# Optimization experiments

Hardware: AMD Instinct MI355X
Metric: run time of the kernel (lower is better)

The kernel has to match this reference:

```python
import jax, jax.numpy as jnp
import numpy as np

ANG = 5
WS = 8
HEADS = 2
REF = 2  # refPos = [2, 2]
NEG_SLOPE = 0.1
EPS = 1e-5


def _rel_pos_index(ws):
    coords = np.stack(np.meshgrid(np.arange(ws), np.arange(ws), indexing='ij'))  # [2,ws,ws]
    cf = coords.reshape(2, -1)
    rel = (cf[:, :, None] - cf[:, None, :]).transpose(1, 2, 0)  # [N,N,2]
    rel[..., 0] += ws - 1
    rel[..., 1] += ws - 1
    rel[..., 0] *= 2 * ws - 1
    return jnp.asarray(rel.sum(-1))  # [N,N] int

REL_IDX = _rel_pos_index(WS)


def _ln(x, g, b):
    m = jnp.mean(x, -1, keepdims=True)
    v = jnp.var(x, -1, keepdims=True)
    return (x - m) * jax.lax.rsqrt(v + EPS) * g + b


def setup_inputs():
    key = jax.random.key(0)
    ks = jax.random.split(key, 12)
    b, an2, c, h, w = 2, 25, 32, 96, 96
    C = 2 * c
    s = 0.02
    mlp_hidden = int(C * 4.0)
    inp = {}
    inp['global_fea'] = jax.random.normal(ks[0], (b, an2, c, h, w), jnp.float32)
    inp['centra_fea'] = jax.random.normal(ks[1], (b, c, h, w), jnp.float32)
    inp['disparity'] = jax.random.uniform(ks[2], (b, 1, h, w), jnp.float32)
    inp['qkv_w'] = jax.random.normal(ks[3], (3 * C, C), jnp.float32) * s
    inp['qkv_b'] = jnp.zeros((3 * C,), jnp.float32)
    inp['proj_w'] = jax.random.normal(ks[4], (C, C), jnp.float32) * s
    inp['proj_b'] = jnp.zeros((C,), jnp.float32)
    inp['rpb_table'] = jax.random.normal(ks[5], ((2 * WS - 1) ** 2, HEADS), jnp.float32) * s
    inp['ln1_g'] = jnp.ones((C,), jnp.float32)
    inp['ln1_b'] = jnp.zeros((C,), jnp.float32)
    inp['ln2_g'] = jnp.ones((C,), jnp.float32)
    inp['ln2_b'] = jnp.zeros((C,), jnp.float32)
    inp['fc1_w'] = jax.random.normal(ks[6], (mlp_hidden, C), jnp.float32) * s
    inp['fc1_b'] = jnp.zeros((mlp_hidden,), jnp.float32)
    inp['fc2_w'] = jax.random.normal(ks[7], (C, mlp_hidden), jnp.float32) * s
    inp['fc2_b'] = jnp.zeros((C,), jnp.float32)
    inp['conv_w'] = jax.random.normal(ks[8], (c, C), jnp.float32) * s  # 1x1 conv kernel squeezed
    inp['conv_b'] = jnp.zeros((c,), jnp.float32)
    return inp


def _warp(centra_fea, disparity):
    # back-projection: bilinear warp of the central (2,2) view to all ANG*ANG views
    b, c, h, w = centra_fea.shape
    d = disparity[:, 0]  # [b,h,w]
    ys, xs = jnp.meshgrid(jnp.arange(h, dtype=jnp.float32), jnp.arange(w, dtype=jnp.float32), indexing='ij')
    offs = jnp.asarray([[u - REF, v - REF] for u in range(ANG) for v in range(ANG)], jnp.float32)  # [an2,2]
    sy = ys[None, None] + d[:, None] * offs[None, :, 0, None, None]  # [b,an2,h,w]
    sx = xs[None, None] + d[:, None] * offs[None, :, 1, None, None]
    x0f = jnp.floor(sx)
    y0f = jnp.floor(sy)
    wx = sx - x0f
    wy = sy - y0f
    x0 = jnp.clip(x0f.astype(jnp.int32), 0, w - 1)
    x1 = jnp.clip(x0 + 1, 0, w - 1)
    y0 = jnp.clip(y0f.astype(jnp.int32), 0, h - 1)
    y1 = jnp.clip(y0 + 1, 0, h - 1)
    flat = centra_fea.reshape(b, c, h * w)
    an2 = ANG * ANG

    def gather(yi, xi):
        idx = (yi * w + xi).reshape(b, 1, -1)  # [b,1,an2*h*w]
        g = jnp.take_along_axis(flat, jnp.broadcast_to(idx, (b, c, an2 * h * w)), axis=2)
        return g.reshape(b, c, an2, h, w).transpose(0, 2, 1, 3, 4)  # [b,an2,c,h,w]

    wx_ = wx[:, :, None]
    wy_ = wy[:, :, None]
    return ((1 - wy_) * (1 - wx_) * gather(y0, x0) + (1 - wy_) * wx_ * gather(y0, x1)
            + wy_ * (1 - wx_) * gather(y1, x0) + wy_ * wx_ * gather(y1, x1))


def reference(global_fea, centra_fea, disparity, qkv_w, qkv_b, proj_w, proj_b, rpb_table,
              ln1_g, ln1_b, ln2_g, ln2_b, fc1_w, fc1_b, fc2_w, fc2_b, conv_w, conv_b):
    b, an2, c, h, w = global_fea.shape
    warped = _warp(centra_fea, disparity)
    x = jnp.concatenate([global_fea, warped], axis=2)  # [b,an2,2c,h,w]
    C = 2 * c
    B = b * an2
    # 'b an2 c h w -> (b an2) (h w) c'
    x = x.reshape(B, C, h, w).transpose(0, 2, 3, 1).reshape(B, h * w, C)
    # --- Swin transformer block (shift_size=0, iteration_idx=0) ---
    shortcut = x
    xn = _ln(x, ln1_g, ln1_b).reshape(B, h, w, C)
    nh, nw = h // WS, w // WS
    xw = xn.reshape(B, nh, WS, nw, WS, C).transpose(0, 1, 3, 2, 4, 5).reshape(B * nh * nw, WS * WS, C)
    nwins, N = xw.shape[0], WS * WS
    hd = C // HEADS
    qkv = (xw @ qkv_w.T + qkv_b).reshape(nwins, N, 3, HEADS, hd).transpose(2, 0, 3, 1, 4)
    q, k, v = qkv[0], qkv[1], qkv[2]  # [nwins, heads, N, hd]
    scale = hd ** -0.5
    attn = jnp.einsum('whnd,whmd->whnm', q * scale, k)
    bias = rpb_table[REL_IDX].transpose(2, 0, 1)  # [heads,N,N]
    attn = jax.nn.softmax(attn + bias[None], axis=-1)
    out = jnp.einsum('whnm,whmd->whnd', attn, v).transpose(0, 2, 1, 3).reshape(nwins, N, C)
    out = out @ proj_w.T + proj_b
    out = out.reshape(B, nh, nw, WS, WS, C).transpose(0, 1, 3, 2, 4, 5).reshape(B, h * w, C)
    x = shortcut + out
    xm = _ln(x, ln2_g, ln2_b)
    xm = jax.nn.gelu(xm @ fc1_w.T + fc1_b, approximate=False) @ fc2_w.T + fc2_b
    x = x + xm
    # '(b an2) (h w) c -> (b an2) c h w' then 1x1 conv fuse + LeakyReLU(0.1)
    x = x.reshape(B, h, w, C)
    y = jnp.einsum('bhwc,oc->bohw', x, conv_w) + conv_b[None, :, None, None]
    y = jnp.where(y >= 0, y, NEG_SLOPE * y)
    return y.reshape(b, an2, c, h, w)
```

## Files before the change

kernel.cpp:

```cpp
#include <hip/hip_runtime.h>
#include <hip/hip_bf16.h>
#include <math.h>

#define W_    96
#define HW_   9216
#define NWIN_ 144

typedef __attribute__((ext_vector_type(4))) float          f32x4;
typedef __attribute__((ext_vector_type(8))) __bf16         bf16x8;
typedef __attribute__((ext_vector_type(8))) unsigned short u16x8;

#define MFMA(a,b,c) __builtin_amdgcn_mfma_f32_16x16x32_bf16((a),(b),(c),0,0,0)

#define WOFF_QKV  0
#define WOFF_PROJ 12288
#define WOFF_FC1  16384
#define WOFF_FC2  32768
#define WOFF_CONV 49152
#define WTOT      51200
#define BIAS_N    8192
#define POFF_QKVB  0
#define POFF_PROJB 192
#define POFF_FC1B  256
#define POFF_FC2B  512
#define POFF_CONVB 576
#define POFF_LN1G  1058
#define POFF_LN1B  1122
#define POFF_LN2G  1186
#define POFF_LN2B  1250
#define PTOT       1314

#define LOG2E 1.44269504f

__device__ __forceinline__ float ldin(const void* p, long i, int isbf){
    return isbf ? __bfloat162float(((const __hip_bfloat16*)p)[i]) : ((const float*)p)[i];
}
__device__ __forceinline__ bf16x8 ldbf8(const __bf16* w){
    u16x8 u = *(const u16x8*)w;
    return __builtin_bit_cast(bf16x8, u);
}

__device__ __forceinline__ float gelu_f(float v){
    float t = v*v;
    float s = 2.3022151f + 0.10294372f*t;
    float z = __builtin_amdgcn_exp2f(fminf(v*s, 80.f));
    return v*z*__builtin_amdgcn_rcpf(z + 1.f);
}

__global__ void probe_kernel(const void* ln1g, int* flag){
    if (threadIdx.x == 0){
        unsigned u = *(const unsigned*)ln1g;
        *flag = (u == 0x3F803F80u) ? 1 : 0;
    }
}

__global__ __launch_bounds__(256) void convert_params(
    const int* __restrict__ flag,
    const void* qkvw, const void* qkvb, const void* projw, const void* projb, const void* rpb,
    const void* ln1g, const void* ln1b, const void* ln2g, const void* ln2b,
    const void* fc1w, const void* fc1b, const void* fc2w, const void* fc2b,
    const void* convw, const void* convb,
    __bf16* __restrict__ wbf, float* __restrict__ pf, float* __restrict__ biasf)
{
    const int isbf = *flag;
    int idx = blockIdx.x*256 + threadIdx.x;
    if (idx >= WTOT + PTOT + BIAS_N) return;
    if (idx < WTOT){
        if      (idx < 12288) wbf[WOFF_QKV  + idx]          = (__bf16)ldin(qkvw, idx, isbf);
        else if (idx < 16384) wbf[WOFF_PROJ + (idx-12288)]  = (__bf16)ldin(projw, idx-12288, isbf);
        else if (idx < 32768) wbf[WOFF_FC1  + (idx-16384)]  = (__bf16)ldin(fc1w, idx-16384, isbf);
        else if (idx < 49152) wbf[WOFF_FC2  + (idx-32768)]  = (__bf16)ldin(fc2w, idx-32768, isbf);
        else                  wbf[WOFF_CONV + (idx-49152)]  = (__bf16)ldin(convw, idx-49152, isbf);
    } else if (idx < WTOT + PTOT){
        int p = idx - WTOT;
        if      (p < 192)  pf[POFF_QKVB  + p]        = ldin(qkvb, p, isbf);
        else if (p < 256)  pf[POFF_PROJB + (p-192)]  = ldin(projb, p-192, isbf);
        else if (p < 512)  pf[POFF_FC1B  + (p-256)]  = ldin(fc1b, p-256, isbf);
        else if (p < 576)  pf[POFF_FC2B  + (p-512)]  = ldin(fc2b, p-512, isbf);
        else if (p < 608)  pf[POFF_CONVB + (p-576)]  = ldin(convb, p-576, isbf);
        else if (p < 1058) ;
        else if (p < 1122) pf[POFF_LN1G  + (p-1058)] = ldin(ln1g, p-1058, isbf);
        else if (p < 1186) pf[POFF_LN1B  + (p-1122)] = ldin(ln1b, p-1122, isbf);
        else if (p < 1250) pf[POFF_LN2G  + (p-1186)] = ldin(ln2g, p-1186, isbf);
        else               pf[POFF_LN2B  + (p-1250)] = ldin(ln2b, p-1250, isbf);
    } else {
        int eb = idx - (WTOT + PTOT);
        int r = eb & 3, jt = (eb>>2)&3, h = (eb>>4)&1, cl = (eb>>5)&15, g = (eb>>9)&3, w = (eb>>11)&3;
        int i = w*16 + g*4 + r;
        int j = jt*16 + cl;
        int di = (i>>3)-(j>>3)+7, dj = (i&7)-(j&7)+7;
        biasf[eb] = ldin(rpb, (di*15+dj)*2 + h, isbf) * LOG2E;
    }
}

template<typename T>
__device__ __forceinline__ void phaseA(
    const T* __restrict__ gf, const T* __restrict__ cf, const T* __restrict__ disp,
    float* tile, float* tile2,
    int tid,int b,int a,int wy,int wx,int hw00)
{
    const int p = tid & 63;
    const int ty = p >> 3, tx = p & 7;
    const int y = wy*8 + ty, x = wx*8 + tx;
    float d = (float)disp[(long)b*HW_ + y*W_ + x];
    float dy = (float)(a/5 - 2), dxs = (float)(a%5 - 2);
    float sy = (float)y + d*dy, sx = (float)x + d*dxs;
    float y0f = floorf(sy), x0f = floorf(sx);
    float fy = sy - y0f, fx = sx - x0f;
    int y0 = min(max((int)y0f,0), W_-1);
    int x0 = min(max((int)x0f,0), W_-1);
    int y1 = min(y0+1,W_-1), x1 = min(x0+1,W_-1);
    float w00=(1.f-fy)*(1.f-fx), w01=(1.f-fy)*fx, w10=fy*(1.f-fx), w11=fy*fx;
    long r0 = (long)y0*W_, r1 = (long)y1*W_;
    const int c0 = tid>>6;
    long gbase = (((long)b*25 + a)*32 + c0)*HW_ + hw00 + ty*W_ + tx;
    long cbase = ((long)b*32 + c0)*HW_;
    for (int c = c0; c < 32; c += 4){
        tile[c*67 + p] = (float)gf[gbase];
        float v00 = (float)cf[cbase+r0+x0], v01 = (float)cf[cbase+r0+x1];
        float v10 = (float)cf[cbase+r1+x0], v11 = (float)cf[cbase+r1+x1];
        tile2[c*67 + p] = w00*v00 + w01*v01 + w10*v10 + w11*v11;
        gbase += 4*HW_; cbase += 4*HW_;
    }
}

__global__ __launch_bounds__(256,4) void fused_kernel(
    const int* __restrict__ flag,
    const void* __restrict__ gf, const void* __restrict__ cf, const void* __restrict__ disp,
    const __bf16* __restrict__ wbf, const float* __restrict__ pf,
    const float* __restrict__ biasf,
    void* __restrict__ out)
{
    __shared__ __bf16 xs[64*72];
    __shared__ __bf16 arena[13824];

    const int isbf = *flag;
    const int tid  = threadIdx.x;
    const int lane = tid & 63, wid = tid >> 6;
    const int g = lane >> 4, cl = lane & 15;
    const int bid  = blockIdx.x;
    const int blk  = (bid & 7)*900 + (bid >> 3);
    const int Bidx = blk / NWIN_;
    const int wrem = blk % NWIN_;
    const int wy = wrem / 12, wx = wrem % 12;
    const int b = Bidx / 25, a = Bidx % 25;
    const int hw00 = (wy*8)*W_ + wx*8;
    const int f = wid*16 + cl;

    __bf16* qb  = arena;
    __bf16* kb  = arena + 4608;
    __bf16* xn  = arena + 9216;
    __bf16* vT  = arena + 9216;

    float* tile  = (float*)arena;
    float* tile2 = tile + 2144;

    bf16x8 wq[3][2];
    #pragma unroll
    for (int nt=0;nt<3;++nt)
        #pragma unroll
        for (int ks=0;ks<2;++ks)
            wq[nt][ks] = ldbf8(wbf + WOFF_QKV + (long)(nt*64 + f)*64 + ks*32 + 8*g);

    if (isbf) phaseA((const __hip_bfloat16*)gf, (const __hip_bfloat16*)cf,
                     (const __hip_bfloat16*)disp, tile, tile2, tid,b,a,wy,wx,hw00);
    else      phaseA((const float*)gf, (const float*)cf,
                     (const float*)disp, tile, tile2, tid,b,a,wy,wx,hw00);
    __syncthreads();

    {
        const int t = tid>>2, quad = tid&3;
        float v[16]; float sum=0.f, sq=0.f;
        #pragma unroll
        for (int j=0;j<16;++j){
            int c = quad*16+j;
            float val = (c<32) ? tile[c*67 + t] : tile2[(c-32)*67 + t];
            v[j]=val; sum+=val; sq+=val*val;
        }
        sum += __shfl_xor(sum,1); sq += __shfl_xor(sq,1);
        sum += __shfl_xor(sum,2); sq += __shfl_xor(sq,2);
        float m  = sum*(1.f/64.f);
        float rs = rsqrtf(sq*(1.f/64.f) - m*m + 1e-5f);
        bf16x8 s0,s1,n0,n1;
        #pragma unroll
        for (int j=0;j<8;++j){
            int c0 = quad*16+j, c1 = quad*16+8+j;
            s0[j] = (__bf16)v[j];
            s1[j] = (__bf16)v[8+j];
            n0[j] = (__bf16)((v[j]  -m)*rs*pf[POFF_LN1G+c0] + pf[POFF_LN1B+c0]);
            n1[j] = (__bf16)((v[8+j]-m)*rs*pf[POFF_LN1G+c1] + pf[POFF_LN1B+c1]);
        }
        *(bf16x8*)(xs + t*72 + quad*16)     = s0;
        *(bf16x8*)(xs + t*72 + quad*16 + 8) = s1;
        *(bf16x8*)(xn + t*72 + quad*16)     = n0;
        *(bf16x8*)(xn + t*72 + quad*16 + 8) = n1;
    }
    __syncthreads();

    {
        bf16x8 af[4][2];
        #pragma unroll
        for (int m=0;m<4;++m)
            #pragma unroll
            for (int ks=0;ks<2;++ks)
                af[m][ks] = *(const bf16x8*)(xn + (16*m+cl)*72 + ks*32 + 8*g);
        __syncthreads();
        f32x4 acc[3][4];
        #pragma unroll
        for (int nt=0;nt<3;++nt)
            #pragma unroll
            for (int m=0;m<4;++m) acc[nt][m] = (f32x4){0.f,0.f,0.f,0.f};
        __builtin_amdgcn_s_setprio(1);
        #pragma unroll
        for (int ks=0;ks<2;++ks)
            #pragma unroll
            for (int nt=0;nt<3;++nt)
                #pragma unroll
                for (int m=0;m<4;++m) acc[nt][m] = MFMA(af[m][ks], wq[nt][ks], acc[nt][m]);
        __builtin_amdgcn_s_setprio(0);
        float bq = pf[POFF_QKVB + f], bk2 = pf[POFF_QKVB + 64 + f], bv2 = pf[POFF_QKVB + 128 + f];
        #pragma unroll
        for (int m=0;m<4;++m)
            #pragma unroll
            for (int r=0;r<4;++r){
                int t = 16*m + 4*g + r;
                qb[t*72 + f] = (__bf16)((acc[0][m][r] + bq)*0.25502224f);
                kb[t*72 + f] = (__bf16)(acc[1][m][r] + bk2);
                vT[f*72 + t] = (__bf16)(acc[2][m][r] + bv2);
            }
    }
    __syncthreads();

    const int strip = wid*16;
    f32x4 sc[2][4];
    {
        const float* bb = biasf + ((wid*4+g)*16+cl)*32;
        bf16x8 aq0 = *(const bf16x8*)(qb + (strip+cl)*72 + 8*g);
        bf16x8 aq1 = *(const bf16x8*)(qb + (strip+cl)*72 + 32 + 8*g);
        __builtin_amdgcn_s_setprio(1);
        #pragma unroll
        for (int h=0;h<2;++h)
            #pragma unroll
            for (int jt=0;jt<4;++jt){
                bf16x8 bk = *(const bf16x8*)(kb + (jt*16+cl)*72 + 32*h + 8*g);
                f32x4 cini = *(const f32x4*)(bb + (h*4+jt)*4);
                sc[h][jt] = MFMA(h?aq1:aq0, bk, cini);
            }
        __builtin_amdgcn_s_setprio(0);
    }
    __syncthreads();

    __bf16* pbuf = qb;
    __bf16* ob   = kb;
    #pragma unroll
    for (int h=0;h<2;++h){
        float inv[4];
        #pragma unroll
        for (int r=0;r<4;++r){
            float s=0.f;
            #pragma unroll
            for (int jt=0;jt<4;++jt){
                float e = __builtin_amdgcn_exp2f(sc[h][jt][r]);
                sc[h][jt][r]=e; s+=e;
            }
            s += __shfl_xor(s,1); s += __shfl_xor(s,2);
            s += __shfl_xor(s,4); s += __shfl_xor(s,8);
            inv[r] = __builtin_amdgcn_rcpf(s);
        }
        #pragma unroll
        for (int jt=0;jt<4;++jt)
            #pragma unroll
            for (int r=0;r<4;++r)
                pbuf[(strip+4*g+r)*72 + jt*16+cl] = (__bf16)sc[h][jt][r];
        bf16x8 ap0 = *(const bf16x8*)(pbuf + (strip+cl)*72 + 8*g);
        bf16x8 ap1 = *(const bf16x8*)(pbuf + (strip+cl)*72 + 32 + 8*g);
        f32x4 ov[2];
        ov[0] = (f32x4){0.f,0.f,0.f,0.f};
        ov[1] = (f32x4){0.f,0.f,0.f,0.f};
        __builtin_amdgcn_s_setprio(1);
        #pragma unroll
        for (int ks=0;ks<2;++ks)
            #pragma unroll
            for (int dt=0;dt<2;++dt){
                bf16x8 bv = *(const bf16x8*)(vT + (32*h + dt*16 + cl)*72 + ks*32 + 8*g);
                ov[dt] = MFMA(ks?ap1:ap0, bv, ov[dt]);
            }
        __builtin_amdgcn_s_setprio(0);
        #pragma unroll
        for (int dt=0;dt<2;++dt)
            #pragma unroll
            for (int r=0;r<4;++r)
                ob[(strip+4*g+r)*72 + 32*h + dt*16 + cl] = (__bf16)(ov[dt][r]*inv[r]);
    }
    __syncthreads();

    {
        f32x4 pacc[4];
        #pragma unroll
        for (int m=0;m<4;++m) pacc[m] = (f32x4){0.f,0.f,0.f,0.f};
        __builtin_amdgcn_s_setprio(1);
        #pragma unroll
        for (int ks=0;ks<2;++ks){
            bf16x8 bw = ldbf8(wbf + WOFF_PROJ + (long)f*64 + ks*32 + 8*g);
            #pragma unroll
            for (int m=0;m<4;++m){
                bf16x8 ao = *(const bf16x8*)(ob + (16*m+cl)*72 + ks*32 + 8*g);
                pacc[m] = MFMA(ao, bw, pacc[m]);
            }
        }
        __builtin_amdgcn_s_setprio(0);
        float pbias = pf[POFF_PROJB + f];
        #pragma unroll
        for (int m=0;m<4;++m)
            #pragma unroll
            for (int r=0;r<4;++r){
                int t = 16*m + 4*g + r;
                float y = (float)xs[t*72 + f] + pacc[m][r] + pbias;
                xs[t*72 + f] = (__bf16)y;
            }
    }
    __syncthreads();

    __bf16* xn2 = arena + 9216;
    {
        const int t = tid>>2, quad = tid&3;
        bf16x8 r0 = *(const bf16x8*)(xs + t*72 + quad*16);
        bf16x8 r1 = *(const bf16x8*)(xs + t*72 + quad*16 + 8);
        float v[16]; float sum=0.f, sq=0.f;
        #pragma unroll
        for (int j=0;j<8;++j){ v[j] = (float)r0[j]; v[8+j] = (float)r1[j]; }
        #pragma unroll
        for (int j=0;j<16;++j){ sum += v[j]; sq += v[j]*v[j]; }
        sum += __shfl_xor(sum,1); sq += __shfl_xor(sq,1);
        sum += __shfl_xor(sum,2); sq += __shfl_xor(sq,2);
        float m  = sum*(1.f/64.f);
        float rs = rsqrtf(sq*(1.f/64.f) - m*m + 1e-5f);
        bf16x8 n0,n1;
        #pragma unroll
        for (int j=0;j<8;++j){
            int c0 = quad*16+j, c1 = quad*16+8+j;
            n0[j] = (__bf16)((v[j]  -m)*rs*pf[POFF_LN2G+c0] + pf[POFF_LN2B+c0]);
            n1[j] = (__bf16)((v[8+j]-m)*rs*pf[POFF_LN2G+c1] + pf[POFF_LN2B+c1]);
        }
        *(bf16x8*)(xn2 + t*72 + quad*16)     = n0;
        *(bf16x8*)(xn2 + t*72 + quad*16 + 8) = n1;
    }
    __syncthreads();

    __bf16* hb = arena;
    {
        bf16x8 af[4][2];
        #pragma unroll
        for (int m=0;m<4;++m)
            #pragma unroll
            for (int ks=0;ks<2;++ks)
                af[m][ks] = *(const bf16x8*)(xn2 + (16*m+cl)*72 + ks*32 + 8*g);
        f32x4 acc2[4];
        #pragma unroll
        for (int m=0;m<4;++m) acc2[m] = (f32x4){0.f,0.f,0.f,0.f};
        #pragma unroll
        for (int half=0; half<2; ++half){
            f32x4 a1[2][4];
            #pragma unroll
            for (int nt=0;nt<2;++nt)
                #pragma unroll
                for (int m=0;m<4;++m) a1[nt][m] = (f32x4){0.f,0.f,0.f,0.f};
            __builtin_amdgcn_s_setprio(1);
            #pragma unroll
            for (int ks=0;ks<2;++ks)
                #pragma unroll
                for (int nt=0;nt<2;++nt){
                    int hrow = half*128 + (2*wid+nt)*16 + cl;
                    bf16x8 bw = ldbf8(wbf + WOFF_FC1 + (long)hrow*64 + ks*32 + 8*g);
                    #pragma unroll
                    for (int m=0;m<4;++m) a1[nt][m] = MFMA(af[m][ks], bw, a1[nt][m]);
                }
            __builtin_amdgcn_s_setprio(0);
            #pragma unroll
            for (int nt=0;nt<2;++nt){
                int hrow = half*128 + (2*wid+nt)*16 + cl;
                float hbias = pf[POFF_FC1B + hrow];
                #pragma unroll
                for (int m=0;m<4;++m)
                    #pragma unroll
                    for (int r=0;r<4;++r){
                        float vv = gelu_f(a1[nt][m][r] + hbias);
                        hb[(16*m+4*g+r)*136 + (2*wid+nt)*16 + cl] = (__bf16)vv;
                    }
            }
            __syncthreads();
            __builtin_amdgcn_s_setprio(1);
            #pragma unroll
            for (int ks=0;ks<4;++ks){
                bf16x8 bw = ldbf8(wbf + WOFF_FC2 + (long)f*256 + half*128 + ks*32 + 8*g);
                #pragma unroll
                for (int m=0;m<4;++m){
                    bf16x8 ah = *(const bf16x8*)(hb + (16*m+cl)*136 + ks*32 + 8*g);
                    acc2[m] = MFMA(ah, bw, acc2[m]);
                }
            }
            __builtin_amdgcn_s_setprio(0);
            __syncthreads();
        }
        float b2 = pf[POFF_FC2B + f];
        #pragma unroll
        for (int m=0;m<4;++m)
            #pragma unroll
            for (int r=0;r<4;++r){
                int t = 16*m + 4*g + r;
                float y = (float)xs[t*72 + f] + acc2[m][r] + b2;
                xs[t*72 + f] = (__bf16)y;
            }
    }
    __syncthreads();

    {
        const int nt = wid & 1, mh = wid >> 1;
        f32x4 ca[2];
        ca[0] = (f32x4){0.f,0.f,0.f,0.f};
        ca[1] = (f32x4){0.f,0.f,0.f,0.f};
        #pragma unroll
        for (int ks=0;ks<2;++ks){
            bf16x8 bw = ldbf8(wbf + WOFF_CONV + (long)(nt*16+cl)*64 + ks*32 + 8*g);
            #pragma unroll
            for (int mm=0;mm<2;++mm){
                bf16x8 afr = *(const bf16x8*)(xs + (16*(mh*2+mm)+cl)*72 + ks*32 + 8*g);
                ca[mm] = MFMA(afr, bw, ca[mm]);
            }
        }
        float cbias = pf[POFF_CONVB + nt*16 + cl];
        float* outs = (float*)arena;
        #pragma unroll
        for (int mm=0;mm<2;++mm)
            #pragma unroll
            for (int r=0;r<4;++r){
                int t = 16*(mh*2+mm) + 4*g + r;
                float vv = ca[mm][r] + cbias;
                vv = (vv >= 0.f) ? vv : 0.1f*vv;
                outs[(nt*16+cl)*68 + t] = vv;
            }
    }
    __syncthreads();

    {
        const int co = tid >> 3, seg = tid & 7;
        const float* outs = (const float*)arena;
        long obase = ((long)Bidx*32 + co)*HW_ + hw00 + (long)seg*W_;
        if (isbf){
            bf16x8 vb;
            #pragma unroll
            for (int j=0;j<8;++j) vb[j] = (__bf16)outs[co*68 + seg*8 + j];
            *(bf16x8*)((__hip_bfloat16*)out + obase) = vb;
        } else {
            f32x4 va, vb2;
            #pragma unroll
            for (int j=0;j<4;++j){ va[j] = outs[co*68 + seg*8 + j]; vb2[j] = outs[co*68 + seg*8 + 4 + j]; }
            *(f32x4*)((float*)out + obase)     = va;
            *(f32x4*)((float*)out + obase + 4) = vb2;
        }
    }
}

extern "C" void kernel_launch(void* const* d_in, const int* in_sizes, int n_in,
                              void* d_out, int out_size, void* d_ws, size_t ws_size,
                              hipStream_t stream)
{
    const void* gf    = d_in[0];
    const void* cf    = d_in[1];
    const void* disp  = d_in[2];
    const void* qkvw  = d_in[3];
    const void* qkvb  = d_in[4];
    const void* projw = d_in[5];
    const void* projb = d_in[6];
    const void* rpb   = d_in[7];
    const void* ln1g  = d_in[8];
    const void* ln1b  = d_in[9];
    const void* ln2g  = d_in[10];
    const void* ln2b  = d_in[11];
    const void* fc1w  = d_in[12];
    const void* fc1b  = d_in[13];
    const void* fc2w  = d_in[14];
    const void* fc2b  = d_in[15];
    const void* convw = d_in[16];
    const void* convb = d_in[17];

    int*    flag  = (int*)d_ws;
    float*  pf    = (float*)((char*)d_ws + 512);
    __bf16* wbf   = (__bf16*)((char*)d_ws + 8192);
    float*  biasf = (float*)((char*)d_ws + 131072);

    probe_kernel<<<1, 64, 0, stream>>>(ln1g, flag);

    const int cgrid = (WTOT + PTOT + BIAS_N + 255)/256;
    convert_params<<<cgrid,256,0,stream>>>(flag,
        qkvw,qkvb,projw,projb,rpb,ln1g,ln1b,ln2g,ln2b,
        fc1w,fc1b,fc2w,fc2b,convw,convb, wbf, pf, biasf);

    fused_kernel<<<7200,256,0,stream>>>(flag, gf, cf, disp, wbf, pf, biasf, d_out);
}
```

Before: 344.9 us.

## Swizzle LDS tiles instead of padding to cut shared memory and raise occupancy

Swaps the padded row strides (72/136) in every shared-memory buffer for XOR-swizzled dense layouts. LDS per block shrinks, which lets the launch bound move from 4 to 5 blocks per CU. It also drops the s_setprio hints around the MFMA loops and adds a barrier before the LN1 stores, because the smaller arena now overlaps the phase-A tile. The swizzle adds index arithmetic and must keep every producer and consumer consistent, and the higher occupancy target may force register spills.

```diff
diff --git a/kernel.cpp b/kernel.cpp
--- a/kernel.cpp
+++ b/kernel.cpp
@@ -38,6 +38,13 @@
 __device__ __forceinline__ bf16x8 ldbf8(const __bf16* w){
     u16x8 u = *(const u16x8*)w;
     return __builtin_bit_cast(bf16x8, u);
+}
+
+__device__ __forceinline__ int SW64(int t, int c){
+    return t*64 + ((((c>>3) ^ (t&7))<<3) | (c&7));
+}
+__device__ __forceinline__ int SWH(int t, int h){
+    return t*128 + ((((h>>3) ^ (t&15))<<3) | (h&7));
 }
 
 __device__ __forceinline__ float gelu_f(float v){
@@ -124,15 +131,15 @@
     }
 }
 
-__global__ __launch_bounds__(256,4) void fused_kernel(
+__global__ __launch_bounds__(256,5) void fused_kernel(
     const int* __restrict__ flag,
     const void* __restrict__ gf, const void* __restrict__ cf, const void* __restrict__ disp,
     const __bf16* __restrict__ wbf, const float* __restrict__ pf,
     const float* __restrict__ biasf,
     void* __restrict__ out)
 {
-    __shared__ __bf16 xs[64*72];
-    __shared__ __bf16 arena[13824];
+    __shared__ __bf16 xsb[4096];
+    __shared__ __bf16 arena[12288];
 
     const int isbf = *flag;
     const int tid  = threadIdx.x;
@@ -148,9 +155,9 @@
     const int f = wid*16 + cl;
 
     __bf16* qb  = arena;
-    __bf16* kb  = arena + 4608;
-    __bf16* xn  = arena + 9216;
-    __bf16* vT  = arena + 9216;
+    __bf16* kb  = arena + 4096;
+    __bf16* xn  = arena + 8192;
+    __bf16* vT  = arena + 8192;
 
     float* tile  = (float*)arena;
     float* tile2 = tile + 2144;
@@ -190,10 +197,11 @@
             n0[j] = (__bf16)((v[j]  -m)*rs*pf[POFF_LN1G+c0] + pf[POFF_LN1B+c0]);
             n1[j] = (__bf16)((v[8+j]-m)*rs*pf[POFF_LN1G+c1] + pf[POFF_LN1B+c1]);
         }
-        *(bf16x8*)(xs + t*72 + quad*16)     = s0;
-        *(bf16x8*)(xs + t*72 + quad*16 + 8) = s1;
-        *(bf16x8*)(xn + t*72 + quad*16)     = n0;
-        *(bf16x8*)(xn + t*72 + quad*16 + 8) = n1;
+        __syncthreads();
+        *(bf16x8*)(xsb + SW64(t, quad*16))   = s0;
+        *(bf16x8*)(xsb + SW64(t, quad*16+8)) = s1;
+        *(bf16x8*)(xn  + SW64(t, quad*16))   = n0;
+        *(bf16x8*)(xn  + SW64(t, quad*16+8)) = n1;
     }
     __syncthreads();
 
@@ -203,30 +211,28 @@
         for (int m=0;m<4;++m)
             #pragma unroll
             for (int ks=0;ks<2;++ks)
-                af[m][ks] = *(const bf16x8*)(xn + (16*m+cl)*72 + ks*32 + 8*g);
+                af[m][ks] = *(const bf16x8*)(xn + SW64(16*m+cl, ks*32 + 8*g));
         __syncthreads();
         f32x4 acc[3][4];
         #pragma unroll
         for (int nt=0;nt<3;++nt)
             #pragma unroll
             for (int m=0;m<4;++m) acc[nt][m] = (f32x4){0.f,0.f,0.f,0.f};
-        __builtin_amdgcn_s_setprio(1);
         #pragma unroll
         for (int ks=0;ks<2;++ks)
             #pragma unroll
             for (int nt=0;nt<3;++nt)
                 #pragma unroll
                 for (int m=0;m<4;++m) acc[nt][m] = MFMA(af[m][ks], wq[nt][ks], acc[nt][m]);
-        __builtin_amdgcn_s_setprio(0);
         float bq = pf[POFF_QKVB + f], bk2 = pf[POFF_QKVB + 64 + f], bv2 = pf[POFF_QKVB + 128 + f];
         #pragma unroll
         for (int m=0;m<4;++m)
             #pragma unroll
             for (int r=0;r<4;++r){
                 int t = 16*m + 4*g + r;
-                qb[t*72 + f] = (__bf16)((acc[0][m][r] + bq)*0.25502224f);
-                kb[t*72 + f] = (__bf16)(acc[1][m][r] + bk2);
-                vT[f*72 + t] = (__bf16)(acc[2][m][r] + bv2);
+                qb[SW64(t, f)] = (__bf16)((acc[0][m][r] + bq)*0.25502224f);
+                kb[SW64(t, f)] = (__bf16)(acc[1][m][r] + bk2);
+                vT[SW64(f, t)] = (__bf16)(acc[2][m][r] + bv2);
             }
     }
     __syncthreads();
@@ -235,18 +241,16 @@
     f32x4 sc[2][4];
     {
         const float* bb = biasf + ((wid*4+g)*16+cl)*32;
-        bf16x8 aq0 = *(const bf16x8*)(qb + (strip+cl)*72 + 8*g);
-        bf16x8 aq1 = *(const bf16x8*)(qb + (strip+cl)*72 + 32 + 8*g);
-        __builtin_amdgcn_s_setprio(1);
+        bf16x8 aq0 = *(const bf16x8*)(qb + SW64(strip+cl, 8*g));
+        bf16x8 aq1 = *(const bf16x8*)(qb + SW64(strip+cl, 32 + 8*g));
         #pragma unroll
         for (int h=0;h<2;++h)
             #pragma unroll
             for (int jt=0;jt<4;++jt){
-                bf16x8 bk = *(const bf16x8*)(kb + (jt*16+cl)*72 + 32*h + 8*g);
+                bf16x8 bk = *(const bf16x8*)(kb + SW64(jt*16+cl, 32*h + 8*g));
                 f32x4 cini = *(const f32x4*)(bb + (h*4+jt)*4);
                 sc[h][jt] = MFMA(h?aq1:aq0, bk, cini);
             }
-        __builtin_amdgcn_s_setprio(0);
     }
     __syncthreads();
 
@@ -271,26 +275,24 @@
         for (int jt=0;jt<4;++jt)
             #pragma unroll
             for (int r=0;r<4;++r)
-                pbuf[(strip+4*g+r)*72 + jt*16+cl] = (__bf16)sc[h][jt][r];
-        bf16x8 ap0 = *(const bf16x8*)(pbuf + (strip+cl)*72 + 8*g);
-        bf16x8 ap1 = *(const bf16x8*)(pbuf + (strip+cl)*72 + 32 + 8*g);
+                pbuf[SW64(strip+4*g+r, jt*16+cl)] = (__bf16)sc[h][jt][r];
+        bf16x8 ap0 = *(const bf16x8*)(pbuf + SW64(strip+cl, 8*g));
+        bf16x8 ap1 = *(const bf16x8*)(pbuf + SW64(strip+cl, 32 + 8*g));
         f32x4 ov[2];
         ov[0] = (f32x4){0.f,0.f,0.f,0.f};
         ov[1] = (f32x4){0.f,0.f,0.f,0.f};
-        __builtin_amdgcn_s_setprio(1);
         #pragma unroll
         for (int ks=0;ks<2;++ks)
             #pragma unroll
             for (int dt=0;dt<2;++dt){
-                bf16x8 bv = *(const bf16x8*)(vT + (32*h + dt*16 + cl)*72 + ks*32 + 8*g);
+                bf16x8 bv = *(const bf16x8*)(vT + SW64(32*h + dt*16 + cl, ks*32 + 8*g));
                 ov[dt] = MFMA(ks?ap1:ap0, bv, ov[dt]);
             }
-        __builtin_amdgcn_s_setprio(0);
         #pragma unroll
         for (int dt=0;dt<2;++dt)
             #pragma unroll
             for (int r=0;r<4;++r)
-                ob[(strip+4*g+r)*72 + 32*h + dt*16 + cl] = (__bf16)(ov[dt][r]*inv[r]);
+                ob[SW64(strip+4*g+r, 32*h + dt*16 + cl)] = (__bf16)(ov[dt][r]*inv[r]);
     }
     __syncthreads();
 
@@ -298,34 +300,33 @@
         f32x4 pacc[4];
         #pragma unroll
         for (int m=0;m<4;++m) pacc[m] = (f32x4){0.f,0.f,0.f,0.f};
-        __builtin_amdgcn_s_setprio(1);
         #pragma unroll
         for (int ks=0;ks<2;++ks){
             bf16x8 bw = ldbf8(wbf + WOFF_PROJ + (long)f*64 + ks*32 + 8*g);
             #pragma unroll
             for (int m=0;m<4;++m){
-                bf16x8 ao = *(const bf16x8*)(ob + (16*m+cl)*72 + ks*32 + 8*g);
+                bf16x8 ao = *(const bf16x8*)(ob + SW64(16*m+cl, ks*32 + 8*g));
                 pacc[m] = MFMA(ao, bw, pacc[m]);
             }
         }
-        __builtin_amdgcn_s_setprio(0);
         float pbias = pf[POFF_PROJB + f];
         #pragma unroll
         for (int m=0;m<4;++m)
             #pragma unroll
             for (int r=0;r<4;++r){
                 int t = 16*m + 4*g + r;
-                float y = (float)xs[t*72 + f] + pacc[m][r] + pbias;
-                xs[t*72 + f] = (__bf16)y;
-            }
-    }
-    __syncthreads();
-
-    __bf16* xn2 = arena + 9216;
+                int xi = SW64(t, f);
+                float y = (float)xsb[xi] + pacc[m][r] + pbias;
+                xsb[xi] = (__bf16)y;
+            }
+    }
+    __syncthreads();
+
+    __bf16* xn2 = arena + 8192;
     {
         const int t = tid>>2, quad = tid&3;
-        bf16x8 r0 = *(const bf16x8*)(xs + t*72 + quad*16);
-        bf16x8 r1 = *(const bf16x8*)(xs + t*72 + quad*16 + 8);
+        bf16x8 r0 = *(const bf16x8*)(xsb + SW64(t, quad*16));
+        bf16x8 r1 = *(const bf16x8*)(xsb + SW64(t, quad*16+8));
         float v[16]; float sum=0.f, sq=0.f;
         #pragma unroll
         for (int j=0;j<8;++j){ v[j] = (float)r0[j]; v[8+j] = (float)r1[j]; }
@@ -342,8 +343,8 @@
             n0[j] = (__bf16)((v[j]  -m)*rs*pf[POFF_LN2G+c0] + pf[POFF_LN2B+c0]);
             n1[j] = (__bf16)((v[8+j]-m)*rs*pf[POFF_LN2G+c1] + pf[POFF_LN2B+c1]);
         }
-        *(bf16x8*)(xn2 + t*72 + quad*16)     = n0;
-        *(bf16x8*)(xn2 + t*72 + quad*16 + 8) = n1;
+        *(bf16x8*)(xn2 + SW64(t, quad*16))   = n0;
+        *(bf16x8*)(xn2 + SW64(t, quad*16+8)) = n1;
     }
     __syncthreads();
 
@@ -354,7 +355,7 @@
         for (int m=0;m<4;++m)
             #pragma unroll
             for (int ks=0;ks<2;++ks)
-                af[m][ks] = *(const bf16x8*)(xn2 + (16*m+cl)*72 + ks*32 + 8*g);
+                af[m][ks] = *(const bf16x8*)(xn2 + SW64(16*m+cl, ks*32 + 8*g));
         f32x4 acc2[4];
         #pragma unroll
         for (int m=0;m<4;++m) acc2[m] = (f32x4){0.f,0.f,0.f,0.f};
@@ -365,7 +366,6 @@
             for (int nt=0;nt<2;++nt)
                 #pragma unroll
                 for (int m=0;m<4;++m) a1[nt][m] = (f32x4){0.f,0.f,0.f,0.f};
-            __builtin_amdgcn_s_setprio(1);
             #pragma unroll
             for (int ks=0;ks<2;++ks)
                 #pragma unroll
@@ -375,7 +375,6 @@
                     #pragma unroll
                     for (int m=0;m<4;++m) a1[nt][m] = MFMA(af[m][ks], bw, a1[nt][m]);
                 }
-            __builtin_amdgcn_s_setprio(0);
             #pragma unroll
             for (int nt=0;nt<2;++nt){
                 int hrow = half*128 + (2*wid+nt)*16 + cl;
@@ -385,21 +384,19 @@
                     #pragma unroll
                     for (int r=0;r<4;++r){
                         float vv = gelu_f(a1[nt][m][r] + hbias);
-                        hb[(16*m+4*g+r)*136 + (2*wid+nt)*16 + cl] = (__bf16)vv;
+                        hb[SWH(16*m+4*g+r, (2*wid+nt)*16 + cl)] = (__bf16)vv;
                     }
             }
             __syncthreads();
-            __builtin_amdgcn_s_setprio(1);
             #pragma unroll
             for (int ks=0;ks<4;++ks){
                 bf16x8 bw = ldbf8(wbf + WOFF_FC2 + (long)f*256 + half*128 + ks*32 + 8*g);
                 #pragma unroll
                 for (int m=0;m<4;++m){
-                    bf16x8 ah = *(const bf16x8*)(hb + (16*m+cl)*136 + ks*32 + 8*g);
+                    bf16x8 ah = *(const bf16x8*)(hb + SWH(16*m+cl, ks*32 + 8*g));
                     acc2[m] = MFMA(ah, bw, acc2[m]);
                 }
             }
-            __builtin_amdgcn_s_setprio(0);
             __syncthreads();
         }
         float b2 = pf[POFF_FC2B + f];
@@ -408,8 +405,9 @@
             #pragma unroll
             for (int r=0;r<4;++r){
                 int t = 16*m + 4*g + r;
-                float y = (float)xs[t*72 + f] + acc2[m][r] + b2;
-                xs[t*72 + f] = (__bf16)y;
+                int xi = SW64(t, f);
+                float y = (float)xsb[xi] + acc2[m][r] + b2;
+                xsb[xi] = (__bf16)y;
             }
     }
     __syncthreads();
@@ -424,7 +422,7 @@
             bf16x8 bw = ldbf8(wbf + WOFF_CONV + (long)(nt*16+cl)*64 + ks*32 + 8*g);
             #pragma unroll
             for (int mm=0;mm<2;++mm){
-                bf16x8 afr = *(const bf16x8*)(xs + (16*(mh*2+mm)+cl)*72 + ks*32 + 8*g);
+                bf16x8 afr = *(const bf16x8*)(xsb + SW64(16*(mh*2+mm)+cl, ks*32 + 8*g));
                 ca[mm] = MFMA(afr, bw, ca[mm]);
             }
         }
```

Result: slower. 616.1 us (+78.6%).
